# Kernel tuning notes

Measured on AMD Instinct MI355X. Metric: run time of the kernel, lower is better.

## Reference

```python
import jax, jax.numpy as jnp
import numpy as np

REGION = (4, 4, 4)
NHEAD = 4
HEAD_DIM = 64
SCALE = HEAD_DIM ** -0.5
NUM_MODALITIES = 4


def _grid2seq(x, region, nhead):
    # x: [B, C, H, W, D] -> [B, nhead, n_regions, region_cube, head_dim]
    B, C, H, W, D = x.shape
    rh, rw, rd = H // region[0], W // region[1], D // region[2]
    hd = C // nhead
    x = x.reshape(B, nhead, hd, rh, region[0], rw, region[1], rd, region[2])
    x = x.transpose(0, 1, 3, 5, 7, 4, 6, 8, 2)  # bmchpwqdr -> bmhwdpqrc
    return x.reshape(B, nhead, rh * rw * rd, region[0] * region[1] * region[2], hd), rh, rw, rd


def _seq2grid(x, rh, rw, rd, region):
    # x: [B, nhead, n_regions, region_cube, head_dim] -> [B, C, H, W, D]
    B, nhead, nreg, rc, hd = x.shape
    x = x.reshape(B, nhead, rh, rw, rd, region[0], region[1], region[2], hd)
    x = x.transpose(0, 1, 8, 2, 5, 3, 6, 4, 7)  # bmhwdpqrc -> bmchpwqdr
    return x.reshape(B, nhead * hd, rh * region[0], rw * region[1], rd * region[2])


def _gather_regions(kv_seq, rg):
    # kv_seq: [B, H, kvN, kc, hd], rg: [B, H, qN, topk] -> [B, H, qN, topk, kc, hd]
    return jax.vmap(jax.vmap(lambda k, g: k[g]))(kv_seq, rg)


def setup_inputs() -> dict:
    key = jax.random.key(0)
    ks = jax.random.split(key, 20)
    shp = (2, 256, 16, 16, 16)
    inp = {"mask": jnp.ones((2, 4), dtype=jnp.int32)}
    names = [f"{p}{i}" for p in ("q", "k", "v") for i in range(4)]
    for n, kk in zip(names, ks[:12]):
        inp[n] = jax.random.normal(kk, shp, dtype=jnp.float32)
    for i, kk in zip(range(4), ks[12:16]):
        inp[f"rg{i}"] = jax.random.randint(kk, (2, 4, 64, 4), 0, 64, dtype=jnp.int32)
    return inp


def reference(mask, q0, q1, q2, q3, k0, k1, k2, k3, v0, v1, v2, v3, rg0, rg1, rg2, rg3):
    qs = [q0, q1, q2, q3]
    ks = [k0, k1, k2, k3]
    vs = [v0, v1, v2, v3]
    rgs = [rg0, rg1, rg2, rg3]

    q_seq, rh, rw, rd = zip(*[(g[0], g[1], g[2], g[3]) for g in [_grid2seq(q, REGION, NHEAD) for q in qs]])
    rh, rw, rd = rh[0], rw[0], rd[0]

    key_parts, val_parts = [], []
    for k_, v_, rg_ in zip(ks, vs, rgs):
        kseq, _, _, _ = _grid2seq(k_, REGION, NHEAD)
        vseq, _, _, _ = _grid2seq(v_, REGION, NHEAD)
        B, H, kvN, kc, hd = kseq.shape
        qN = rg_.shape[2]
        kg = _gather_regions(kseq, rg_).reshape(B, H, qN, -1, hd)  # [B,H,qN,topk*kc,hd]
        vg = _gather_regions(vseq, rg_).reshape(B, H, qN, -1, hd)
        key_parts.append(kg)
        val_parts.append(vg)
    key_g = jnp.concatenate(key_parts, axis=-2)  # [B,H,qN, M*topk*kc, hd]
    value_g = jnp.concatenate(val_parts, axis=-2)

    N = key_g.shape[-2]
    rep = N // NUM_MODALITIES
    mask_full = jnp.repeat(mask[:, None, None, None, :], rep, axis=-1)  # [B,1,1,1,N]

    outs = []
    for q in q_seq:
        attn = jnp.einsum("bhnqc,bhnkc->bhnqk", q * SCALE, key_g)
        attn = jnp.where(mask_full == 0, -jnp.inf, attn)
        attn = jax.nn.softmax(attn, axis=-1)
        o = jnp.einsum("bhnqk,bhnkc->bhnqc", attn, value_g)
        outs.append(_seq2grid(o, rh, rw, rd, REGION))
    return jnp.stack(outs, axis=0)  # [M, B, C, H, W, D]
```

## Files before the change

kernel.cpp:

```cpp
#include <hip/hip_runtime.h>
#include <hip/hip_bf16.h>

typedef short v8s __attribute__((ext_vector_type(8)));
typedef short v4s __attribute__((ext_vector_type(4)));
typedef float v4f __attribute__((ext_vector_type(4)));

#define LDK 72
#define SCALE_LOG2E 0.18033688f

struct MMRAParams {
    const float* q[4];
    const float* k[4];
    const float* v[4];
    const int*   rg[4];
    const int*   mask;
    float*       out;
};

__device__ __forceinline__ unsigned pkbf(float a, float b) {
    unsigned r;
    asm("v_cvt_pk_bf16_f32 %0, %1, %2" : "=v"(r) : "v"(a), "v"(b));
    return r;
}

__device__ __forceinline__ float fexp2(float x) {
#if __has_builtin(__builtin_amdgcn_exp2f)
    return __builtin_amdgcn_exp2f(x);
#else
    return exp2f(x);
#endif
}

__device__ __forceinline__ v4f mfma16(v4s a, v4s b, v4f c) {
#if __has_builtin(__builtin_amdgcn_mfma_f32_16x16x16bf16_1k)
    return __builtin_amdgcn_mfma_f32_16x16x16bf16_1k(a, b, c, 0, 0, 0);
#elif __has_builtin(__builtin_amdgcn_mfma_f32_16x16x16_bf16)
    return __builtin_amdgcn_mfma_f32_16x16x16_bf16(a, b, c, 0, 0, 0);
#else
    asm("v_mfma_f32_16x16x16_bf16 %0, %1, %2, %0" : "+v"(c) : "v"(a), "v"(b));
    return c;
#endif
}

__global__ __launch_bounds__(256, 2)
void mmra_attn(MMRAParams P) {
    const int bid = blockIdx.x;
    const int h = bid & 3;
    const int b = (bid >> 2) & 1;
    const int n = bid >> 3;
    const int H0 = ((n >> 4) & 3) << 2;
    const int W0 = ((n >> 2) & 3) << 2;
    const int D0 = (n & 3) << 2;

    const int tid  = threadIdx.x;
    const int wave = tid >> 6;
    const int lane = tid & 63;
    const int l15  = lane & 15;
    const int quad = lane >> 4;

    __shared__ __align__(16) ushort SMEM[36864];

    const int bh_base = (b * 256 + h * 64) * 4096;
    const int rgbase  = ((b * 4 + h) * 64 + n) * 4;

    const bool actm[4] = { P.mask[b * 4 + 0] != 0, P.mask[b * 4 + 1] != 0,
                           P.mask[b * 4 + 2] != 0, P.mask[b * 4 + 3] != 0 };

    auto kptr = [&](int m) { return (m == 0) ? P.k[0] : (m == 1) ? P.k[1] : (m == 2) ? P.k[2] : P.k[3]; };
    auto vptr = [&](int m) { return (m == 0) ? P.v[0] : (m == 1) ? P.v[1] : (m == 2) ? P.v[2] : P.v[3]; };
    auto rptr = [&](int m) { return (m == 0) ? P.rg[0] : (m == 1) ? P.rg[1] : (m == 2) ? P.rg[2] : P.rg[3]; };

    unsigned long long clist = 0ull; int nc = 0;
    for (int m = 0; m < 4; ++m) {
        if (actm[m]) {
            #pragma unroll
            for (int s = 0; s < 4; ++s) { clist |= ((unsigned long long)(m * 4 + s)) << (4 * nc); ++nc; }
        }
    }
    auto chunkAt = [&](int i) { return (int)((clist >> (4 * i)) & 15); };

    float4 pkf[4], pvf[4];
    auto prefetch = [&](int cj) {
        const int mod = cj >> 2, j = cj & 3;
        const int g = rptr(mod)[rgbase + j] & 63;
        const int goff = (((g >> 4) & 3) << 10) + (((g >> 2) & 3) << 6) + ((g & 3) << 2);
        const float* ks = kptr(mod);
        const float* vs = vptr(mod);
        const int off0 = bh_base + lane * 4096 + goff;
        #pragma unroll
        for (int i = 0; i < 4; ++i) {
            const int pq = wave * 4 + i;
            const int off = off0 + (pq >> 2) * 256 + (pq & 3) * 16;
            pkf[i] = *(const float4*)(ks + off);
            pvf[i] = *(const float4*)(vs + off);
        }
    };

    auto stage = [&](int buf) {
        ushort* Kb = SMEM + buf * 9216;
        ushort* Vb = Kb + 4608;
        #pragma unroll
        for (int i = 0; i < 4; ++i) {
            const int pq = wave * 4 + i;
            unsigned k01 = pkbf(pkf[i].x, pkf[i].y);
            unsigned k23 = pkbf(pkf[i].z, pkf[i].w);
            ushort* kb = &Kb[(pq * 4) * LDK + lane];
            kb[0 * LDK] = (ushort)k01;
            kb[1 * LDK] = (ushort)(k01 >> 16);
            kb[2 * LDK] = (ushort)k23;
            kb[3 * LDK] = (ushort)(k23 >> 16);
            uint2 vv;
            vv.x = pkbf(pvf[i].x, pvf[i].y);
            vv.y = pkbf(pvf[i].z, pvf[i].w);
            *(uint2*)&Vb[lane * LDK + pq * 4] = vv;
        }
    };

    prefetch(chunkAt(0));

    v8s qfrag[4][2];
    {
        ushort* qbuf = SMEM + wave * 4608;
        const float* qsrc = (wave == 0) ? P.q[0] : (wave == 1) ? P.q[1] : (wave == 2) ? P.q[2] : P.q[3];
        #pragma unroll
        for (int rb = 0; rb < 4; ++rb) {
            #pragma unroll
            for (int i = 0; i < 4; ++i) {
                int off = bh_base + lane * 4096 + (H0 + rb) * 256 + (W0 + i) * 16 + D0;
                float4 cv = *(const float4*)(qsrc + off);
                unsigned q01 = pkbf(cv.x * SCALE_LOG2E, cv.y * SCALE_LOG2E);
                unsigned q23 = pkbf(cv.z * SCALE_LOG2E, cv.w * SCALE_LOG2E);
                ushort* qb = &qbuf[(rb * 16 + i * 4) * LDK + lane];
                qb[0 * LDK] = (ushort)q01;
                qb[1 * LDK] = (ushort)(q01 >> 16);
                qb[2 * LDK] = (ushort)q23;
                qb[3 * LDK] = (ushort)(q23 >> 16);
            }
        }
        __asm__ volatile("s_waitcnt lgkmcnt(0)" ::: "memory");
        #pragma unroll
        for (int rb = 0; rb < 4; ++rb) {
            qfrag[rb][0] = *(const v8s*)&qbuf[(rb * 16 + l15) * LDK + quad * 8];
            qfrag[rb][1] = *(const v8s*)&qbuf[(rb * 16 + l15) * LDK + 32 + quad * 8];
        }
    }
    __syncthreads();
    stage(0);
    if (nc > 1) { prefetch(chunkAt(1)); stage(1); }
    if (nc > 2) prefetch(chunkAt(2));
    __syncthreads();

    v4f  oacc[4][4];
    float lrow[4];
    #pragma unroll
    for (int mt = 0; mt < 4; ++mt) {
        lrow[mt] = 0.f;
        #pragma unroll
        for (int t = 0; t < 4; ++t) oacc[mt][t] = (v4f){0.f, 0.f, 0.f, 0.f};
    }

    auto computeChunk = [&](const ushort* Kb, const ushort* Vb) {
        v8s kf[4][2];
        #pragma unroll
        for (int nt = 0; nt < 4; ++nt) {
            kf[nt][0] = *(const v8s*)&Kb[(nt * 16 + l15) * LDK + quad * 8];
            kf[nt][1] = *(const v8s*)&Kb[(nt * 16 + l15) * LDK + 32 + quad * 8];
        }
        uint2 pa[4][4];
        #pragma unroll
        for (int mt = 0; mt < 4; ++mt) {
            float sv[4][4];
            __builtin_amdgcn_s_setprio(1);
            #pragma unroll
            for (int nt = 0; nt < 4; ++nt) {
                v4f acc = (v4f){0.f, 0.f, 0.f, 0.f};
                acc = __builtin_amdgcn_mfma_f32_16x16x32_bf16(kf[nt][0], qfrag[mt][0], acc, 0, 0, 0);
                acc = __builtin_amdgcn_mfma_f32_16x16x32_bf16(kf[nt][1], qfrag[mt][1], acc, 0, 0, 0);
                #pragma unroll
                for (int r = 0; r < 4; ++r) sv[nt][r] = acc[r];
            }
            __builtin_amdgcn_s_setprio(0);
            float rsum = 0.f;
            #pragma unroll
            for (int nt = 0; nt < 4; ++nt) {
                float p0 = fexp2(sv[nt][0]);
                float p1 = fexp2(sv[nt][1]);
                float p2 = fexp2(sv[nt][2]);
                float p3 = fexp2(sv[nt][3]);
                rsum += (p0 + p1) + (p2 + p3);
                pa[mt][nt].x = pkbf(p0, p1);
                pa[mt][nt].y = pkbf(p2, p3);
            }
            lrow[mt] += rsum;
        }
        __builtin_amdgcn_s_setprio(1);
        #pragma unroll
        for (int t = 0; t < 4; ++t) {
            #pragma unroll
            for (int nt = 0; nt < 4; ++nt) {
                v4s vf = *(const v4s*)&Vb[(t * 16 + l15) * LDK + nt * 16 + quad * 4];
                #pragma unroll
                for (int mt = 0; mt < 4; ++mt)
                    oacc[mt][t] = mfma16(__builtin_bit_cast(v4s, pa[mt][nt]), vf, oacc[mt][t]);
            }
        }
        __builtin_amdgcn_s_setprio(0);
    };

    #pragma unroll 1
    for (int j = 0; j < nc; j += 2) {
        const int rb = j & 2;
        const bool more = (j + 2 < nc);
        if (more) stage(rb ^ 2);
        if (more) prefetch(chunkAt(j + 3));
        computeChunk(SMEM + rb * 9216, SMEM + rb * 9216 + 4608);
        if (more) stage((rb ^ 2) + 1);
        if (j + 4 < nc) prefetch(chunkAt(j + 4));
        computeChunk(SMEM + (rb + 1) * 9216, SMEM + (rb + 1) * 9216 + 4608);
        __syncthreads();
    }

    const int obase = (wave * 2 + b) * 1048576 + h * 64 * 4096;
    #pragma unroll
    for (int mt = 0; mt < 4; ++mt) {
        float lq = lrow[mt];
        lq += __shfl_xor(lq, 16);
        lq += __shfl_xor(lq, 32);
        const float invq = 1.0f / lq;
        float inv_row[4];
        #pragma unroll
        for (int r = 0; r < 4; ++r)
            inv_row[r] = __shfl(invq, (quad << 4) | (quad * 4 + r));
        #pragma unroll
        for (int t = 0; t < 4; ++t) {
            float4 ov;
            ov.x = oacc[mt][t][0] * inv_row[0];
            ov.y = oacc[mt][t][1] * inv_row[1];
            ov.z = oacc[mt][t][2] * inv_row[2];
            ov.w = oacc[mt][t][3] * inv_row[3];
            int off = obase + (t * 16 + l15) * 4096 + (H0 + mt) * 256 + (W0 + quad) * 16 + D0;
            *(float4*)(P.out + off) = ov;
        }
    }
}

extern "C" void kernel_launch(void* const* d_in, const int* in_sizes, int n_in,
                              void* d_out, int out_size, void* d_ws, size_t ws_size,
                              hipStream_t stream) {
    (void)in_sizes; (void)n_in; (void)out_size; (void)d_ws; (void)ws_size;
    MMRAParams P;
    P.mask = (const int*)d_in[0];
    for (int i = 0; i < 4; ++i) {
        P.q[i]  = (const float*)d_in[1 + i];
        P.k[i]  = (const float*)d_in[5 + i];
        P.v[i]  = (const float*)d_in[9 + i];
        P.rg[i] = (const int*)d_in[13 + i];
    }
    P.out = (float*)d_out;
    hipLaunchKernelGGL(mmra_attn, dim3(512), dim3(256), 0, stream, P);
}
```

Baseline: 243.8 us.

## Split query tiles across eight waves and switch to single-chunk double buffering

Doubles the block to 512 threads so each wave handles two of the four query row tiles for one modality instead of all four, halving per-wave accumulator and fragment registers. K/V staging is spread over eight waves, and the pipeline changes from four LDS buffers processed in pairs to two buffers with one chunk per iteration, halving shared memory. The aim is higher occupancy and more latency hiding, at the cost of one barrier per chunk instead of one per two chunks, and K fragments now loaded from LDS twice as often overall.

```diff
diff --git a/kernel.cpp b/kernel.cpp
--- a/kernel.cpp
+++ b/kernel.cpp
@@ -42,7 +42,7 @@
 #endif
 }
 
-__global__ __launch_bounds__(256, 2)
+__global__ __launch_bounds__(512, 4)
 void mmra_attn(MMRAParams P) {
     const int bid = blockIdx.x;
     const int h = bid & 3;
@@ -54,11 +54,13 @@
 
     const int tid  = threadIdx.x;
     const int wave = tid >> 6;
+    const int qm   = wave >> 1;
+    const int mth  = wave & 1;
     const int lane = tid & 63;
     const int l15  = lane & 15;
     const int quad = lane >> 4;
 
-    __shared__ __align__(16) ushort SMEM[36864];
+    __shared__ __align__(16) ushort SMEM[18432];
 
     const int bh_base = (b * 256 + h * 64) * 4096;
     const int rgbase  = ((b * 4 + h) * 64 + n) * 4;
@@ -79,7 +81,7 @@
     }
     auto chunkAt = [&](int i) { return (int)((clist >> (4 * i)) & 15); };
 
-    float4 pkf[4], pvf[4];
+    float4 pkf[2], pvf[2];
     auto prefetch = [&](int cj) {
         const int mod = cj >> 2, j = cj & 3;
         const int g = rptr(mod)[rgbase + j] & 63;
@@ -88,8 +90,8 @@
         const float* vs = vptr(mod);
         const int off0 = bh_base + lane * 4096 + goff;
         #pragma unroll
-        for (int i = 0; i < 4; ++i) {
-            const int pq = wave * 4 + i;
+        for (int i = 0; i < 2; ++i) {
+            const int pq = wave * 2 + i;
             const int off = off0 + (pq >> 2) * 256 + (pq & 3) * 16;
             pkf[i] = *(const float4*)(ks + off);
             pvf[i] = *(const float4*)(vs + off);
@@ -100,8 +102,8 @@
         ushort* Kb = SMEM + buf * 9216;
         ushort* Vb = Kb + 4608;
         #pragma unroll
-        for (int i = 0; i < 4; ++i) {
-            const int pq = wave * 4 + i;
+        for (int i = 0; i < 2; ++i) {
+            const int pq = wave * 2 + i;
             unsigned k01 = pkbf(pkf[i].x, pkf[i].y);
             unsigned k23 = pkbf(pkf[i].z, pkf[i].w);
             ushort* kb = &Kb[(pq * 4) * LDK + lane];
@@ -118,19 +120,20 @@
 
     prefetch(chunkAt(0));
 
-    v8s qfrag[4][2];
+    v8s qfrag[2][2];
     {
-        ushort* qbuf = SMEM + wave * 4608;
-        const float* qsrc = (wave == 0) ? P.q[0] : (wave == 1) ? P.q[1] : (wave == 2) ? P.q[2] : P.q[3];
-        #pragma unroll
-        for (int rb = 0; rb < 4; ++rb) {
+        ushort* qbuf = SMEM + wave * 2304;
+        const float* qsrc = (qm == 0) ? P.q[0] : (qm == 1) ? P.q[1] : (qm == 2) ? P.q[2] : P.q[3];
+        #pragma unroll
+        for (int m2 = 0; m2 < 2; ++m2) {
+            const int rb = mth * 2 + m2;
             #pragma unroll
             for (int i = 0; i < 4; ++i) {
                 int off = bh_base + lane * 4096 + (H0 + rb) * 256 + (W0 + i) * 16 + D0;
                 float4 cv = *(const float4*)(qsrc + off);
                 unsigned q01 = pkbf(cv.x * SCALE_LOG2E, cv.y * SCALE_LOG2E);
                 unsigned q23 = pkbf(cv.z * SCALE_LOG2E, cv.w * SCALE_LOG2E);
-                ushort* qb = &qbuf[(rb * 16 + i * 4) * LDK + lane];
+                ushort* qb = &qbuf[(m2 * 16 + i * 4) * LDK + lane];
                 qb[0 * LDK] = (ushort)q01;
                 qb[1 * LDK] = (ushort)(q01 >> 16);
                 qb[2 * LDK] = (ushort)q23;
@@ -139,43 +142,51 @@
         }
         __asm__ volatile("s_waitcnt lgkmcnt(0)" ::: "memory");
         #pragma unroll
-        for (int rb = 0; rb < 4; ++rb) {
-            qfrag[rb][0] = *(const v8s*)&qbuf[(rb * 16 + l15) * LDK + quad * 8];
-            qfrag[rb][1] = *(const v8s*)&qbuf[(rb * 16 + l15) * LDK + 32 + quad * 8];
+        for (int m2 = 0; m2 < 2; ++m2) {
+            qfrag[m2][0] = *(const v8s*)&qbuf[(m2 * 16 + l15) * LDK + quad * 8];
+            qfrag[m2][1] = *(const v8s*)&qbuf[(m2 * 16 + l15) * LDK + 32 + quad * 8];
         }
     }
     __syncthreads();
     stage(0);
-    if (nc > 1) { prefetch(chunkAt(1)); stage(1); }
-    if (nc > 2) prefetch(chunkAt(2));
+    if (nc > 1) prefetch(chunkAt(1));
     __syncthreads();
 
-    v4f  oacc[4][4];
-    float lrow[4];
+    v4f  oacc[2][4];
+    float lrow[2];
     #pragma unroll
-    for (int mt = 0; mt < 4; ++mt) {
-        lrow[mt] = 0.f;
-        #pragma unroll
-        for (int t = 0; t < 4; ++t) oacc[mt][t] = (v4f){0.f, 0.f, 0.f, 0.f};
-    }
-
-    auto computeChunk = [&](const ushort* Kb, const ushort* Vb) {
+    for (int m2 = 0; m2 < 2; ++m2) {
+        lrow[m2] = 0.f;
+        #pragma unroll
+        for (int t = 0; t < 4; ++t) oacc[m2][t] = (v4f){0.f, 0.f, 0.f, 0.f};
+    }
+
+    int cur = 0;
+    #pragma unroll 1
+    for (int i = 0; i < nc; ++i) {
+        if (i + 1 < nc) {
+            stage(cur ^ 1);
+            if (i + 2 < nc) prefetch(chunkAt(i + 2));
+        }
+        const ushort* Kb = SMEM + cur * 9216;
+        const ushort* Vb = Kb + 4608;
+
         v8s kf[4][2];
         #pragma unroll
         for (int nt = 0; nt < 4; ++nt) {
             kf[nt][0] = *(const v8s*)&Kb[(nt * 16 + l15) * LDK + quad * 8];
             kf[nt][1] = *(const v8s*)&Kb[(nt * 16 + l15) * LDK + 32 + quad * 8];
         }
-        uint2 pa[4][4];
-        #pragma unroll
-        for (int mt = 0; mt < 4; ++mt) {
+        uint2 pa[2][4];
+        #pragma unroll
+        for (int m2 = 0; m2 < 2; ++m2) {
             float sv[4][4];
             __builtin_amdgcn_s_setprio(1);
             #pragma unroll
             for (int nt = 0; nt < 4; ++nt) {
                 v4f acc = (v4f){0.f, 0.f, 0.f, 0.f};
-                acc = __builtin_amdgcn_mfma_f32_16x16x32_bf16(kf[nt][0], qfrag[mt][0], acc, 0, 0, 0);
-                acc = __builtin_amdgcn_mfma_f32_16x16x32_bf16(kf[nt][1], qfrag[mt][1], acc, 0, 0, 0);
+                acc = __builtin_amdgcn_mfma_f32_16x16x32_bf16(kf[nt][0], qfrag[m2][0], acc, 0, 0, 0);
+                acc = __builtin_amdgcn_mfma_f32_16x16x32_bf16(kf[nt][1], qfrag[m2][1], acc, 0, 0, 0);
                 #pragma unroll
                 for (int r = 0; r < 4; ++r) sv[nt][r] = acc[r];
             }
@@ -188,42 +199,33 @@
                 float p2 = fexp2(sv[nt][2]);
                 float p3 = fexp2(sv[nt][3]);
                 rsum += (p0 + p1) + (p2 + p3);
-                pa[mt][nt].x = pkbf(p0, p1);
-                pa[mt][nt].y = pkbf(p2, p3);
-            }
-            lrow[mt] += rsum;
-        }
+                pa[m2][nt].x = pkbf(p0, p1);
+                pa[m2][nt].y = pkbf(p2, p3);
+            }
+            lrow[m2] += rsum;
+        }
+
         __builtin_amdgcn_s_setprio(1);
         #pragma unroll
         for (int t = 0; t < 4; ++t) {
             #pragma unroll
             for (int nt = 0; nt < 4; ++nt) {
                 v4s vf = *(const v4s*)&Vb[(t * 16 + l15) * LDK + nt * 16 + quad * 4];
-                #pragma unroll
-                for (int mt = 0; mt < 4; ++mt)
-                    oacc[mt][t] = mfma16(__builtin_bit_cast(v4s, pa[mt][nt]), vf, oacc[mt][t]);
+                oacc[0][t] = mfma16(__builtin_bit_cast(v4s, pa[0][nt]), vf, oacc[0][t]);
+                oacc[1][t] = mfma16(__builtin_bit_cast(v4s, pa[1][nt]), vf, oacc[1][t]);
             }
         }
         __builtin_amdgcn_s_setprio(0);
-    };
-
-    #pragma unroll 1
-    for (int j = 0; j < nc; j += 2) {
-        const int rb = j & 2;
-        const bool more = (j + 2 < nc);
-        if (more) stage(rb ^ 2);
-        if (more) prefetch(chunkAt(j + 3));
-        computeChunk(SMEM + rb * 9216, SMEM + rb * 9216 + 4608);
-        if (more) stage((rb ^ 2) + 1);
-        if (j + 4 < nc) prefetch(chunkAt(j + 4));
-        computeChunk(SMEM + (rb + 1) * 9216, SMEM + (rb + 1) * 9216 + 4608);
+
         __syncthreads();
-    }
-
-    const int obase = (wave * 2 + b) * 1048576 + h * 64 * 4096;
+        cur ^= 1;
+    }
+
+    const int obase = (qm * 2 + b) * 1048576 + h * 64 * 4096;
     #pragma unroll
-    for (int mt = 0; mt < 4; ++mt) {
-        float lq = lrow[mt];
+    for (int m2 = 0; m2 < 2; ++m2) {
+        const int mt = mth * 2 + m2;
+        float lq = lrow[m2];
         lq += __shfl_xor(lq, 16);
         lq += __shfl_xor(lq, 32);
         const float invq = 1.0f / lq;
@@ -234,10 +236,10 @@
         #pragma unroll
         for (int t = 0; t < 4; ++t) {
             float4 ov;
-            ov.x = oacc[mt][t][0] * inv_row[0];
-            ov.y = oacc[mt][t][1] * inv_row[1];
-            ov.z = oacc[mt][t][2] * inv_row[2];
-            ov.w = oacc[mt][t][3] * inv_row[3];
+            ov.x = oacc[m2][t][0] * inv_row[0];
+            ov.y = oacc[m2][t][1] * inv_row[1];
+            ov.z = oacc[m2][t][2] * inv_row[2];
+            ov.w = oacc[m2][t][3] * inv_row[3];
             int off = obase + (t * 16 + l15) * 4096 + (H0 + mt) * 256 + (W0 + quad) * 16 + D0;
             *(float4*)(P.out + off) = ov;
         }
@@ -257,5 +259,5 @@
         P.rg[i] = (const int*)d_in[13 + i];
     }
     P.out = (float*)d_out;
-    hipLaunchKernelGGL(mmra_attn, dim3(512), dim3(256), 0, stream, P);
-}
+    hipLaunchKernelGGL(mmra_attn, dim3(512), dim3(512), 0, stream, P);
+}
```

New measurement: 334.8 us. +37.3%, slower.
